# Performance work log

Hardware: AMD Instinct MI355X
Metric: run time of the kernel (lower is better)

## Reference

```python
import jax, jax.numpy as jnp
import numpy as np

MLP_WIDTH = 256
NUM_FREQS = 10


def _posenc(x):
    # [x, sin(pi x), cos(pi x), sin(2pi x), cos(2pi x), ...] -> last dim 2*(1+2*NUM_FREQS)=42
    freqs = (2.0 ** jnp.arange(NUM_FREQS, dtype=x.dtype)) * jnp.pi
    parts = [x]
    for f in freqs:
        parts.append(jnp.sin(x * f))
        parts.append(jnp.cos(x * f))
    return jnp.concatenate(parts, axis=-1)


def _bilinear_sample(grid, coords):
    # grid: [B,Hl,Wl,C]; coords: [N,2] in [-1,1], col0=y(dim H), col1=x(dim W).
    # Equivalent to map_coordinates(order=1, mode='reflect') since rescaled coords
    # lie in [0, size-1]; at the upper edge the out-of-range tap has zero weight,
    # so clipping == reflecting.
    Hl, Wl = grid.shape[1], grid.shape[2]
    y = (coords[:, 0] + 1.0) * 0.5 * (Hl - 1)
    x = (coords[:, 1] + 1.0) * 0.5 * (Wl - 1)
    y0 = jnp.floor(y)
    x0 = jnp.floor(x)
    wy = (y - y0)[None, :, None]  # [1,N,1]
    wx = (x - x0)[None, :, None]
    y0i = jnp.clip(y0.astype(jnp.int32), 0, Hl - 1)
    x0i = jnp.clip(x0.astype(jnp.int32), 0, Wl - 1)
    y1i = jnp.clip(y0i + 1, 0, Hl - 1)
    x1i = jnp.clip(x0i + 1, 0, Wl - 1)
    g00 = grid[:, y0i, x0i]  # [B,N,C]
    g01 = grid[:, y0i, x1i]
    g10 = grid[:, y1i, x0i]
    g11 = grid[:, y1i, x1i]
    top = g00 * (1 - wx) + g01 * wx
    bot = g10 * (1 - wx) + g11 * wx
    return top * (1 - wy) + bot * wy


def _forward(feature_grid, context_vector, coords,
             Wc, bc, W0, b0, W1, b1, W2, b2, W3, b3, Wout, bout):
    B, H, W, C = feature_grid.shape
    enc = _posenc(coords)  # [N,42]
    pyramid = [feature_grid] + [
        jax.image.resize(feature_grid, (B, H // 2 ** i, W // 2 ** i, C), 'bilinear')
        for i in range(1, 3)
    ]
    sampled = [_bilinear_sample(g, coords) for g in pyramid]  # each [B,N,C]
    feats = jnp.concatenate(sampled, axis=-1)  # [B,N,3C]
    enc_tiled = jnp.broadcast_to(enc[None], (B,) + enc.shape)
    h = jnp.concatenate([enc_tiled, feats], axis=-1)  # [B,N,42+3C]
    # FiLM projection (shared across all MLP layers, as in the flax module)
    ctx = context_vector @ Wc + bc  # [B, 2*MLP_WIDTH]
    gamma = ctx[:, None, :MLP_WIDTH] + 1.0
    beta = ctx[:, None, MLP_WIDTH:]
    for Wl_, bl_ in ((W0, b0), (W1, b1), (W2, b2), (W3, b3)):
        h = h @ Wl_ + bl_
        h = h * gamma + beta
        h = jax.nn.gelu(h)  # approximate=True, matches flax nn.gelu
    return jnp.tanh(h @ Wout + bout)  # [B,N,3]


def setup_inputs() -> dict:
    key = jax.random.key(0)
    ks = jax.random.split(key, 16)
    B, H, W, C = 8, 64, 64, 64
    N = 16384
    enc_dim = 2 * (1 + 2 * NUM_FREQS)  # 42
    in_dim = enc_dim + 3 * C  # 234
    s = lambda d: 1.0 / np.sqrt(d)
    return {
        'feature_grid': jax.random.normal(ks[0], (B, H, W, C), jnp.float32),
        'context_vector': jax.random.normal(ks[1], (B, C), jnp.float32),
        'coords': jax.random.uniform(ks[2], (N, 2), jnp.float32, -1.0, 1.0),
        'Wc': jax.random.normal(ks[3], (C, 2 * MLP_WIDTH), jnp.float32) * s(C),
        'bc': jnp.zeros((2 * MLP_WIDTH,), jnp.float32),
        'W0': jax.random.normal(ks[4], (in_dim, MLP_WIDTH), jnp.float32) * s(in_dim),
        'b0': jnp.zeros((MLP_WIDTH,), jnp.float32),
        'W1': jax.random.normal(ks[5], (MLP_WIDTH, MLP_WIDTH), jnp.float32) * s(MLP_WIDTH),
        'b1': jnp.zeros((MLP_WIDTH,), jnp.float32),
        'W2': jax.random.normal(ks[6], (MLP_WIDTH, MLP_WIDTH), jnp.float32) * s(MLP_WIDTH),
        'b2': jnp.zeros((MLP_WIDTH,), jnp.float32),
        'W3': jax.random.normal(ks[7], (MLP_WIDTH, MLP_WIDTH), jnp.float32) * s(MLP_WIDTH),
        'b3': jnp.zeros((MLP_WIDTH,), jnp.float32),
        'Wout': jax.random.normal(ks[8], (MLP_WIDTH, 3), jnp.float32) * 0.01,
        'bout': jnp.zeros((3,), jnp.float32),
    }


def reference(feature_grid, context_vector, coords,
              Wc, bc, W0, b0, W1, b1, W2, b2, W3, b3, Wout, bout):
    return _forward(feature_grid, context_vector, coords,
                    Wc, bc, W0, b0, W1, b1, W2, b2, W3, b3, Wout, bout)
```

## Files before the change

kernel.cpp:

```cpp
#include <hip/hip_runtime.h>
#include <math.h>

typedef _Float16 f16x8 __attribute__((ext_vector_type(8)));
typedef float f32x4 __attribute__((ext_vector_type(4)));
typedef float f32x16 __attribute__((ext_vector_type(16)));
typedef unsigned short us8 __attribute__((ext_vector_type(8)));
typedef unsigned short us4 __attribute__((ext_vector_type(4)));

#define PI_F 3.14159265358979323846f

__device__ __forceinline__ unsigned short f2h(float f){
  _Float16 hi = (_Float16)f;
  return __builtin_bit_cast(unsigned short, hi);
}

__device__ __forceinline__ float fast_gelu(float v){
  float u2 = v * v;
  float z  = v * fmaf(u2, 0.03567740814f, 0.7978845608f);
  float e  = __builtin_amdgcn_exp2f(z * 2.885390082f);
  float r  = __builtin_amdgcn_rcpf(e + 1.0f);
  return v - v * r;
}

__device__ __forceinline__ float fast_tanh(float v){
  float e = __builtin_amdgcn_exp2f(v * 2.885390082f);
  float r = __builtin_amdgcn_rcpf(e + 1.0f);
  return 1.0f - 2.0f * r;
}

#define ACOL(rr,cc) (((rr) << 8) + ((cc) ^ ((((rr) & 15)) << 3)))

#define LDW(ptr) __builtin_bit_cast(f16x8, *reinterpret_cast<const us8*>(ptr))

__global__ void pyr_kernel(const float* __restrict__ fg, float* __restrict__ out,
                           int Ho, int Wo, float inv_scale){
  int idx = blockIdx.x * blockDim.x + threadIdx.x;
  int total = 8 * Ho * Wo * 64;
  if (idx >= total) return;
  int c  = idx & 63;
  int xy = idx >> 6;
  int x  = xy % Wo;
  int y  = (xy / Wo) % Ho;
  int b  = xy / (Wo * Ho);
  float cyc = inv_scale * (y + 0.5f) - 0.5f;
  float cxc = inv_scale * (x + 0.5f) - 0.5f;
  int iy0 = (int)ceilf(cyc - inv_scale); if (iy0 < 0) iy0 = 0;
  int iy1 = (int)floorf(cyc + inv_scale); if (iy1 > 63) iy1 = 63;
  int ix0 = (int)ceilf(cxc - inv_scale); if (ix0 < 0) ix0 = 0;
  int ix1 = (int)floorf(cxc + inv_scale); if (ix1 > 63) ix1 = 63;
  float rinv = 1.0f / inv_scale;
  float wxs = 0.0f;
  for (int ix = ix0; ix <= ix1; ++ix){
    float w = 1.0f - fabsf(ix - cxc) * rinv;
    if (w > 0.0f) wxs += w;
  }
  float wys = 0.0f, acc = 0.0f;
  for (int iy = iy0; iy <= iy1; ++iy){
    float wy = 1.0f - fabsf(iy - cyc) * rinv;
    if (wy <= 0.0f) continue;
    wys += wy;
    const float* rowp = fg + (((b * 64) + iy) * 64) * 64 + c;
    for (int ix = ix0; ix <= ix1; ++ix){
      float wx = 1.0f - fabsf(ix - cxc) * rinv;
      if (wx <= 0.0f) continue;
      acc += wy * wx * rowp[ix * 64];
    }
  }
  out[idx] = acc / (wys * wxs);
}

__global__ void pe_kernel(const float* __restrict__ coords,
                          unsigned short* __restrict__ peh){
  int idx = blockIdx.x * 256 + threadIdx.x;
  if (idx >= 16384 * 12) return;
  int n = idx / 12, slot = idx % 12;
  const float cy = coords[2 * n], cx = coords[2 * n + 1];
  if (slot == 0){
    peh[n * 48 + 0] = f2h(cy);
    peh[n * 48 + 1] = f2h(cx);
  } else if (slot <= 10){
    int i = slot - 1;
    float f = PI_F * (float)(1 << i);
    float sy, cyv, sx, cxv;
    sincosf(cy * f, &sy, &cyv);
    sincosf(cx * f, &sx, &cxv);
    peh[n * 48 + 2 + 4 * i] = f2h(sy);
    peh[n * 48 + 3 + 4 * i] = f2h(sx);
    peh[n * 48 + 4 + 4 * i] = f2h(cyv);
    peh[n * 48 + 5 + 4 * i] = f2h(cxv);
  } else {
#pragma unroll
    for (int j = 42; j < 48; ++j) peh[n * 48 + j] = 0;
  }
}

__global__ void prep_wt(const float* __restrict__ W0, const float* __restrict__ W1,
                        const float* __restrict__ W2, const float* __restrict__ W3,
                        unsigned short* __restrict__ WTh){
  int idx = blockIdx.x * 256 + threadIdx.x;
  int l    = idx >> 16;
  int rem  = idx & 65535;
  int cfg  = rem >> 13;
  int ks   = (rem >> 9) & 15;
  int lane = (rem >> 3) & 63;
  int e    = idx & 7;
  int col  = cfg * 32 + (lane & 31);
  int k    = ks * 16 + (lane >> 5) * 8 + e;
  float v;
  if (l == 0){
    int row; bool valid;
    if (k < 42)                 { row = k;     valid = true; }
    else if (k >= 48 && k < 240){ row = k - 6; valid = true; }
    else                        { row = 0;     valid = false; }
    v = valid ? W0[row * 256 + col] : 0.0f;
  } else {
    const float* W = (l == 1) ? W1 : ((l == 2) ? W2 : W3);
    v = W[k * 256 + col];
  }
  WTh[idx] = f2h(v);
}

__global__ void prep_misc(const float* __restrict__ cv, const float* __restrict__ Wc,
                          const float* __restrict__ bc, const float* __restrict__ Wout,
                          float* __restrict__ gamma, float* __restrict__ beta,
                          unsigned short* __restrict__ WoT){
  int idx = blockIdx.x * 256 + threadIdx.x;
  if (idx < 4096){
    int b = idx >> 9, j = idx & 511;
    float a = bc[j];
    for (int c = 0; c < 64; ++c) a += cv[b * 64 + c] * Wc[c * 512 + j];
    if (j < 256) gamma[b * 256 + j] = a + 1.0f;
    else         beta[b * 256 + (j - 256)] = a;
  } else {
    int j = idx - 4096;
    int ks = j >> 9, lane = (j >> 3) & 63, e = j & 7;
    int col = lane & 15;
    int k = ks * 32 + (lane >> 4) * 8 + e;
    float v = (col < 3) ? Wout[k * 3 + col] : 0.0f;
    WoT[j] = f2h(v);
  }
}

__global__ __launch_bounds__(512, 2)
void dec_main(const float* __restrict__ fg, const float* __restrict__ coords,
              const float* __restrict__ p1, const float* __restrict__ p2,
              const unsigned short* __restrict__ WTh,
              const unsigned short* __restrict__ WoT,
              const unsigned short* __restrict__ peh,
              const float* __restrict__ gamma, const float* __restrict__ beta,
              const float* __restrict__ b0, const float* __restrict__ b1,
              const float* __restrict__ b2, const float* __restrict__ b3,
              const float* __restrict__ bout, float* __restrict__ out){
  __shared__ __align__(16) unsigned short Ah0[80 * 256];
  __shared__ __align__(16) unsigned short Ah1[80 * 256];
  __shared__ __align__(16) float Pgs[256];
  __shared__ __align__(16) float C2s[4][256];

  const int t  = threadIdx.x;
  const int bi = blockIdx.x >> 8;
  const int n0 = (blockIdx.x & 255) * 64;

  const int lane = t & 63;
  const int wv   = t >> 6;
  const int l15  = lane & 15;
  const int lg   = lane >> 4;
  const int l31  = lane & 31;
  const int lhi  = lane >> 5;

  const int rg   = wv >> 2;
  const int cg   = wv & 3;
  const int arow = rg * 32 + l31;

  const int b0off = (cg * 2)     * 8192 + lane * 8;
  const int b1off = (cg * 2 + 1) * 8192 + lane * 8;

  if (t < 256){
    const float gm = gamma[bi * 256 + t];
    const float bt = beta[bi * 256 + t];
    Pgs[t] = gm;
    C2s[0][t] = fmaf(b0[t], gm, bt);
    C2s[1][t] = fmaf(b1[t], gm, bt);
    C2s[2][t] = fmaf(b2[t], gm, bt);
    C2s[3][t] = fmaf(b3[t], gm, bt);

    const int r = t >> 2, q = t & 3;
    const int n = n0 + r;
    const float cy = coords[2 * n], cx = coords[2 * n + 1];

    if (q == 0){
      if (peh){
        const unsigned short* ph = peh + (size_t)n * 48;
#pragma unroll
        for (int u = 0; u < 6; ++u){
          us8 vh = *reinterpret_cast<const us8*>(ph + u * 8);
          *reinterpret_cast<us8*>(&Ah0[ACOL(r, u * 8)]) = vh;
        }
      } else {
        float e[48];
        e[0] = cy; e[1] = cx;
#pragma unroll
        for (int i = 0; i < 10; ++i){
          float f = PI_F * (float)(1 << i);
          float sy, cyv, sx, cxv;
          sincosf(cy * f, &sy, &cyv);
          sincosf(cx * f, &sx, &cxv);
          e[2 + 4 * i] = sy;
          e[3 + 4 * i] = sx;
          e[4 + 4 * i] = cyv;
          e[5 + 4 * i] = cxv;
        }
#pragma unroll
        for (int j = 42; j < 48; ++j) e[j] = 0.0f;
#pragma unroll
        for (int u = 0; u < 6; ++u){
          us8 vh;
#pragma unroll
          for (int j = 0; j < 8; ++j) vh[j] = f2h(e[8 * u + j]);
          *reinterpret_cast<us8*>(&Ah0[ACOL(r, u * 8)]) = vh;
        }
      }
    }
    if (q == 1){
      us8 z = {0,0,0,0,0,0,0,0};
      *reinterpret_cast<us8*>(&Ah0[ACOL(r, 240)]) = z;
      *reinterpret_cast<us8*>(&Ah0[ACOL(r, 248)]) = z;
    }

#pragma unroll
    for (int L = 0; L < 3; ++L){
      const int HL = 64 >> L;
      const float* g = (L == 0) ? fg : ((L == 1) ? p1 : p2);
      float yy = (cy + 1.0f) * 0.5f * (HL - 1);
      float xx = (cx + 1.0f) * 0.5f * (HL - 1);
      float y0f = floorf(yy), x0f = floorf(xx);
      float wy = yy - y0f, wx = xx - x0f;
      int y0 = (int)y0f, x0 = (int)x0f;
      y0 = min(max(y0, 0), HL - 1); x0 = min(max(x0, 0), HL - 1);
      int y1 = min(y0 + 1, HL - 1), x1 = min(x0 + 1, HL - 1);
      const int c0 = q * 16;
      const float* g00 = g + (((bi * HL + y0) * HL) + x0) * 64 + c0;
      const float* g01 = g + (((bi * HL + y0) * HL) + x1) * 64 + c0;
      const float* g10 = g + (((bi * HL + y1) * HL) + x0) * 64 + c0;
      const float* g11 = g + (((bi * HL + y1) * HL) + x1) * 64 + c0;
      float w00 = (1 - wy) * (1 - wx), w01 = (1 - wy) * wx;
      float w10 = wy * (1 - wx),       w11 = wy * wx;
      float o[16];
#pragma unroll
      for (int u = 0; u < 4; ++u){
        float4 v0 = *reinterpret_cast<const float4*>(g00 + 4 * u);
        float4 v1 = *reinterpret_cast<const float4*>(g01 + 4 * u);
        float4 v2 = *reinterpret_cast<const float4*>(g10 + 4 * u);
        float4 v3 = *reinterpret_cast<const float4*>(g11 + 4 * u);
        o[4*u+0] = w00*v0.x + w01*v1.x + w10*v2.x + w11*v3.x;
        o[4*u+1] = w00*v0.y + w01*v1.y + w10*v2.y + w11*v3.y;
        o[4*u+2] = w00*v0.z + w01*v1.z + w10*v2.z + w11*v3.z;
        o[4*u+3] = w00*v0.w + w01*v1.w + w10*v2.w + w11*v3.w;
      }
      us8 h0, h1;
#pragma unroll
      for (int j = 0; j < 8; ++j){
        h0[j] = f2h(o[j]);
        h1[j] = f2h(o[8 + j]);
      }
      const int colb = 48 + 64 * L + 16 * q;
      *reinterpret_cast<us8*>(&Ah0[ACOL(r, colb)])     = h0;
      *reinterpret_cast<us8*>(&Ah0[ACOL(r, colb + 8)]) = h1;
    }
  }

  f16x8 bf0[8], bf1[8];
#pragma unroll
  for (int p = 0; p < 8; ++p){
    bf0[p] = LDW(WTh + b0off + p * 512);
    bf1[p] = LDW(WTh + b1off + p * 512);
  }
  __syncthreads();

#pragma unroll
  for (int l = 0; l < 4; ++l){
    const unsigned short* Rh   = (l & 1) ? Ah1 : Ah0;
    unsigned short*       Wh_t = (l & 1) ? Ah0 : Ah1;
    const unsigned short* Wcur = WTh + l * 65536;
    const unsigned short* Wnxt = WTh + (l + 1) * 65536;

    f32x16 accA, accB;
#pragma unroll
    for (int j = 0; j < 16; ++j){ accA[j] = 0.0f; accB[j] = 0.0f; }

#pragma unroll
    for (int ks = 0; ks < 16; ++ks){
      const int cur = ks & 7;
      const int kc = ks * 16 + lhi * 8;
      f16x8 ah  = LDW(&Rh[ACOL(arow, kc)]);
      f16x8 b0v = bf0[cur], b1v = bf1[cur];
      if (ks < 8){
        bf0[cur] = LDW(Wcur + b0off + (ks + 8) * 512);
        bf1[cur] = LDW(Wcur + b1off + (ks + 8) * 512);
      } else if (l < 3){
        bf0[cur] = LDW(Wnxt + b0off + (ks - 8) * 512);
        bf1[cur] = LDW(Wnxt + b1off + (ks - 8) * 512);
      }
      accA = __builtin_amdgcn_mfma_f32_32x32x16_f16(b0v, ah, accA, 0, 0, 0);
      accB = __builtin_amdgcn_mfma_f32_32x32x16_f16(b1v, ah, accB, 0, 0, 0);
    }

#define EPI32(ACC, CF) do { \
      _Pragma("unroll") \
      for (int g = 0; g < 4; ++g){ \
        const int colb = cg * 64 + (CF) * 32 + 4 * lhi + 8 * g; \
        const float4 gm4 = *reinterpret_cast<const float4*>(&Pgs[colb]); \
        const float4 c24 = *reinterpret_cast<const float4*>(&C2s[l][colb]); \
        us4 hh; \
        { float v = fmaf((ACC)[4*g+0], gm4.x, c24.x); hh[0] = f2h(fast_gelu(v)); } \
        { float v = fmaf((ACC)[4*g+1], gm4.y, c24.y); hh[1] = f2h(fast_gelu(v)); } \
        { float v = fmaf((ACC)[4*g+2], gm4.z, c24.z); hh[2] = f2h(fast_gelu(v)); } \
        { float v = fmaf((ACC)[4*g+3], gm4.w, c24.w); hh[3] = f2h(fast_gelu(v)); } \
        *reinterpret_cast<us4*>(&Wh_t[ACOL(arow, colb)]) = hh; \
      } } while(0)
    EPI32(accA, 0);
    EPI32(accB, 1);
#undef EPI32
    __syncthreads();
  }

  if (wv < 4){
    f32x4 ao = (f32x4){0.0f, 0.0f, 0.0f, 0.0f};
#pragma unroll
    for (int ks = 0; ks < 8; ++ks){
      const int kc = ks * 32 + lg * 8;
      f16x8 va = LDW(&Ah0[ACOL(wv * 16 + l15, kc)]);
      f16x8 vb = LDW(&WoT[(ks * 64 + lane) * 8]);
      ao = __builtin_amdgcn_mfma_f32_16x16x32_f16(va, vb, ao, 0, 0, 0);
    }
    if (l15 < 3){
      const float bo = bout[l15];
#pragma unroll
      for (int rg2 = 0; rg2 < 4; ++rg2){
        const int row = wv * 16 + lg * 4 + rg2;
        out[((size_t)bi * 16384 + n0 + row) * 3 + l15] = fast_tanh(ao[rg2] + bo);
      }
    }
  }
}

extern "C" void kernel_launch(void* const* d_in, const int* in_sizes, int n_in,
                              void* d_out, int out_size, void* d_ws, size_t ws_size,
                              hipStream_t stream){
  (void)in_sizes; (void)n_in; (void)out_size;
  const float* fg     = (const float*)d_in[0];
  const float* cv     = (const float*)d_in[1];
  const float* coords = (const float*)d_in[2];
  const float* Wc     = (const float*)d_in[3];
  const float* bc     = (const float*)d_in[4];
  const float* W0     = (const float*)d_in[5];
  const float* b0     = (const float*)d_in[6];
  const float* W1     = (const float*)d_in[7];
  const float* b1     = (const float*)d_in[8];
  const float* W2     = (const float*)d_in[9];
  const float* b2     = (const float*)d_in[10];
  const float* W3     = (const float*)d_in[11];
  const float* b3     = (const float*)d_in[12];
  const float* Wout   = (const float*)d_in[13];
  const float* bout   = (const float*)d_in[14];

  char* ws = (char*)d_ws;
  float*          p1    = (float*)(ws);
  float*          p2    = (float*)(ws + 2097152);
  unsigned short* WTh   = (unsigned short*)(ws + 2621440);
  unsigned short* WoT   = (unsigned short*)(ws + 3670016);
  float*          gam   = (float*)(ws + 3678208);
  float*          bet   = (float*)(ws + 3686400);
  const size_t PEH_OFF = 4194304, PE_END = 5767168;
  bool use_pe = (ws_size >= PE_END);
  unsigned short* PEh = use_pe ? (unsigned short*)(ws + PEH_OFF) : nullptr;
  float* outp = (float*)d_out;

  pyr_kernel<<<dim3(2048), dim3(256), 0, stream>>>(fg, p1, 32, 32, 2.0f);
  pyr_kernel<<<dim3(512),  dim3(256), 0, stream>>>(fg, p2, 16, 16, 4.0f);
  prep_wt  <<<dim3(1024),  dim3(256), 0, stream>>>(W0, W1, W2, W3, WTh);
  prep_misc<<<dim3(32),    dim3(256), 0, stream>>>(cv, Wc, bc, Wout, gam, bet, WoT);
  if (use_pe)
    pe_kernel<<<dim3(768), dim3(256), 0, stream>>>(coords, PEh);
  dec_main <<<dim3(2048),  dim3(512), 0, stream>>>(fg, coords, p1, p2, WTh, WoT,
                                                   PEh,
                                                   gam, bet, b0, b1, b2, b3, bout, outp);
}
```

Measured before the change: 187.5 us.

## Keep MLP activations in registers with per-wave full-width tiles and larger blocks

```diff
diff --git a/kernel.cpp b/kernel.cpp
--- a/kernel.cpp
+++ b/kernel.cpp
@@ -105,15 +105,17 @@
   int lane = (rem >> 3) & 63;
   int e    = idx & 7;
   int col  = cfg * 32 + (lane & 31);
-  int k    = ks * 16 + (lane >> 5) * 8 + e;
   float v;
   if (l == 0){
+    int k = ks * 16 + (lane >> 5) * 8 + e;
     int row; bool valid;
     if (k < 42)                 { row = k;     valid = true; }
     else if (k >= 48 && k < 240){ row = k - 6; valid = true; }
     else                        { row = 0;     valid = false; }
     v = valid ? W0[row * 256 + col] : 0.0f;
   } else {
+    int c_in = ks >> 1, gp = ks & 1;
+    int k = c_in * 32 + gp * 16 + (e >> 2) * 8 + (lane >> 5) * 4 + (e & 3);
     const float* W = (l == 1) ? W1 : ((l == 2) ? W2 : W3);
     v = W[k * 256 + col];
   }
@@ -151,14 +153,13 @@
               const float* __restrict__ b0, const float* __restrict__ b1,
               const float* __restrict__ b2, const float* __restrict__ b3,
               const float* __restrict__ bout, float* __restrict__ out){
-  __shared__ __align__(16) unsigned short Ah0[80 * 256];
-  __shared__ __align__(16) unsigned short Ah1[80 * 256];
+  __shared__ __align__(16) unsigned short T0[256 * 256];
   __shared__ __align__(16) float Pgs[256];
   __shared__ __align__(16) float C2s[4][256];
 
   const int t  = threadIdx.x;
-  const int bi = blockIdx.x >> 8;
-  const int n0 = (blockIdx.x & 255) * 64;
+  const int bi = blockIdx.x >> 6;
+  const int n0 = (blockIdx.x & 63) * 256;
 
   const int lane = t & 63;
   const int wv   = t >> 6;
@@ -166,13 +167,12 @@
   const int lg   = lane >> 4;
   const int l31  = lane & 31;
   const int lhi  = lane >> 5;
-
-  const int rg   = wv >> 2;
-  const int cg   = wv & 3;
-  const int arow = rg * 32 + l31;
-
-  const int b0off = (cg * 2)     * 8192 + lane * 8;
-  const int b1off = (cg * 2 + 1) * 8192 + lane * 8;
+  const int arow = wv * 32 + l31;
+
+  f16x8 Bc[8];
+#pragma unroll
+  for (int c = 0; c < 8; ++c)
+    Bc[c] = LDW(WTh + c * 8192 + lane * 8);
 
   if (t < 256){
     const float gm = gamma[bi * 256 + t];
@@ -182,8 +182,11 @@
     C2s[1][t] = fmaf(b1[t], gm, bt);
     C2s[2][t] = fmaf(b2[t], gm, bt);
     C2s[3][t] = fmaf(b3[t], gm, bt);
-
-    const int r = t >> 2, q = t & 3;
+  }
+
+#pragma unroll
+  for (int pass = 0; pass < 2; ++pass){
+    const int r = pass * 128 + (t >> 2), q = t & 3;
     const int n = n0 + r;
     const float cy = coords[2 * n], cx = coords[2 * n + 1];
 
@@ -193,7 +196,7 @@
 #pragma unroll
         for (int u = 0; u < 6; ++u){
           us8 vh = *reinterpret_cast<const us8*>(ph + u * 8);
-          *reinterpret_cast<us8*>(&Ah0[ACOL(r, u * 8)]) = vh;
+          *reinterpret_cast<us8*>(&T0[ACOL(r, u * 8)]) = vh;
         }
       } else {
         float e[48];
@@ -216,14 +219,14 @@
           us8 vh;
 #pragma unroll
           for (int j = 0; j < 8; ++j) vh[j] = f2h(e[8 * u + j]);
-          *reinterpret_cast<us8*>(&Ah0[ACOL(r, u * 8)]) = vh;
+          *reinterpret_cast<us8*>(&T0[ACOL(r, u * 8)]) = vh;
         }
       }
     }
     if (q == 1){
       us8 z = {0,0,0,0,0,0,0,0};
-      *reinterpret_cast<us8*>(&Ah0[ACOL(r, 240)]) = z;
-      *reinterpret_cast<us8*>(&Ah0[ACOL(r, 248)]) = z;
+      *reinterpret_cast<us8*>(&T0[ACOL(r, 240)]) = z;
+      *reinterpret_cast<us8*>(&T0[ACOL(r, 248)]) = z;
     }
 
 #pragma unroll
@@ -263,72 +266,104 @@
         h1[j] = f2h(o[8 + j]);
       }
       const int colb = 48 + 64 * L + 16 * q;
-      *reinterpret_cast<us8*>(&Ah0[ACOL(r, colb)])     = h0;
-      *reinterpret_cast<us8*>(&Ah0[ACOL(r, colb + 8)]) = h1;
-    }
-  }
-
-  f16x8 bf0[8], bf1[8];
-#pragma unroll
-  for (int p = 0; p < 8; ++p){
-    bf0[p] = LDW(WTh + b0off + p * 512);
-    bf1[p] = LDW(WTh + b1off + p * 512);
+      *reinterpret_cast<us8*>(&T0[ACOL(r, colb)])     = h0;
+      *reinterpret_cast<us8*>(&T0[ACOL(r, colb + 8)]) = h1;
+    }
   }
   __syncthreads();
 
-#pragma unroll
-  for (int l = 0; l < 4; ++l){
-    const unsigned short* Rh   = (l & 1) ? Ah1 : Ah0;
-    unsigned short*       Wh_t = (l & 1) ? Ah0 : Ah1;
-    const unsigned short* Wcur = WTh + l * 65536;
-    const unsigned short* Wnxt = WTh + (l + 1) * 65536;
-
-    f32x16 accA, accB;
-#pragma unroll
-    for (int j = 0; j < 16; ++j){ accA[j] = 0.0f; accB[j] = 0.0f; }
-
-#pragma unroll
-    for (int ks = 0; ks < 16; ++ks){
-      const int cur = ks & 7;
-      const int kc = ks * 16 + lhi * 8;
-      f16x8 ah  = LDW(&Rh[ACOL(arow, kc)]);
-      f16x8 b0v = bf0[cur], b1v = bf1[cur];
-      if (ks < 8){
-        bf0[cur] = LDW(Wcur + b0off + (ks + 8) * 512);
-        bf1[cur] = LDW(Wcur + b1off + (ks + 8) * 512);
-      } else if (l < 3){
-        bf0[cur] = LDW(Wnxt + b0off + (ks - 8) * 512);
-        bf1[cur] = LDW(Wnxt + b1off + (ks - 8) * 512);
-      }
-      accA = __builtin_amdgcn_mfma_f32_32x32x16_f16(b0v, ah, accA, 0, 0, 0);
-      accB = __builtin_amdgcn_mfma_f32_32x32x16_f16(b1v, ah, accB, 0, 0, 0);
-    }
-
-#define EPI32(ACC, CF) do { \
+  f32x16 acc[8];
+  f16x8 actA[16], actB[16];
+
+#define EPI_REG(LIDX, AOUT) do { \
+    _Pragma("unroll") \
+    for (int c = 0; c < 8; ++c){ \
       _Pragma("unroll") \
-      for (int g = 0; g < 4; ++g){ \
-        const int colb = cg * 64 + (CF) * 32 + 4 * lhi + 8 * g; \
-        const float4 gm4 = *reinterpret_cast<const float4*>(&Pgs[colb]); \
-        const float4 c24 = *reinterpret_cast<const float4*>(&C2s[l][colb]); \
-        us4 hh; \
-        { float v = fmaf((ACC)[4*g+0], gm4.x, c24.x); hh[0] = f2h(fast_gelu(v)); } \
-        { float v = fmaf((ACC)[4*g+1], gm4.y, c24.y); hh[1] = f2h(fast_gelu(v)); } \
-        { float v = fmaf((ACC)[4*g+2], gm4.z, c24.z); hh[2] = f2h(fast_gelu(v)); } \
-        { float v = fmaf((ACC)[4*g+3], gm4.w, c24.w); hh[3] = f2h(fast_gelu(v)); } \
-        *reinterpret_cast<us4*>(&Wh_t[ACOL(arow, colb)]) = hh; \
-      } } while(0)
-    EPI32(accA, 0);
-    EPI32(accB, 1);
-#undef EPI32
-    __syncthreads();
-  }
-
-  if (wv < 4){
+      for (int gp = 0; gp < 2; ++gp){ \
+        const int cb2 = c * 32 + 16 * gp + 4 * lhi; \
+        const float4 gmA = *reinterpret_cast<const float4*>(&Pgs[cb2]); \
+        const float4 c2A = *reinterpret_cast<const float4*>(&C2s[LIDX][cb2]); \
+        const float4 gmB = *reinterpret_cast<const float4*>(&Pgs[cb2 + 8]); \
+        const float4 c2B = *reinterpret_cast<const float4*>(&C2s[LIDX][cb2 + 8]); \
+        us8 hv; \
+        hv[0] = f2h(fast_gelu(fmaf(acc[c][8*gp+0], gmA.x, c2A.x))); \
+        hv[1] = f2h(fast_gelu(fmaf(acc[c][8*gp+1], gmA.y, c2A.y))); \
+        hv[2] = f2h(fast_gelu(fmaf(acc[c][8*gp+2], gmA.z, c2A.z))); \
+        hv[3] = f2h(fast_gelu(fmaf(acc[c][8*gp+3], gmA.w, c2A.w))); \
+        hv[4] = f2h(fast_gelu(fmaf(acc[c][8*gp+4], gmB.x, c2B.x))); \
+        hv[5] = f2h(fast_gelu(fmaf(acc[c][8*gp+5], gmB.y, c2B.y))); \
+        hv[6] = f2h(fast_gelu(fmaf(acc[c][8*gp+6], gmB.z, c2B.z))); \
+        hv[7] = f2h(fast_gelu(fmaf(acc[c][8*gp+7], gmB.w, c2B.w))); \
+        (AOUT)[c * 2 + gp] = __builtin_bit_cast(f16x8, hv); \
+      } \
+    } } while(0)
+
+#pragma unroll
+  for (int j = 0; j < 16; ++j){
+#pragma unroll
+    for (int c = 0; c < 8; ++c) acc[c][j] = 0.0f;
+  }
+#pragma unroll
+  for (int ks = 0; ks < 16; ++ks){
+    f16x8 ah = LDW(&T0[ACOL(arow, ks * 16 + lhi * 8)]);
+#pragma unroll
+    for (int c = 0; c < 8; ++c){
+      f16x8 b = Bc[c];
+      if (ks < 15) Bc[c] = LDW(WTh + c * 8192 + (ks + 1) * 512 + lane * 8);
+      else         Bc[c] = LDW(WTh + 65536 + c * 8192 + lane * 8);
+      acc[c] = __builtin_amdgcn_mfma_f32_32x32x16_f16(b, ah, acc[c], 0, 0, 0);
+    }
+  }
+  EPI_REG(0, actA);
+
+#define LAYER_REG(LIDX, AIN, AOUT) do { \
+    _Pragma("unroll") \
+    for (int j = 0; j < 16; ++j){ \
+      _Pragma("unroll") \
+      for (int c = 0; c < 8; ++c) acc[c][j] = 0.0f; \
+    } \
+    _Pragma("unroll") \
+    for (int ks = 0; ks < 16; ++ks){ \
+      f16x8 ah = (AIN)[ks]; \
+      _Pragma("unroll") \
+      for (int c = 0; c < 8; ++c){ \
+        f16x8 b = Bc[c]; \
+        if (ks < 15) \
+          Bc[c] = LDW(WTh + (LIDX) * 65536 + c * 8192 + (ks + 1) * 512 + lane * 8); \
+        else if ((LIDX) < 3) \
+          Bc[c] = LDW(WTh + ((LIDX) + 1) * 65536 + c * 8192 + lane * 8); \
+        acc[c] = __builtin_amdgcn_mfma_f32_32x32x16_f16(b, ah, acc[c], 0, 0, 0); \
+      } \
+    } \
+    EPI_REG(LIDX, AOUT); \
+  } while(0)
+
+  LAYER_REG(1, actA, actB);
+  LAYER_REG(2, actB, actA);
+  LAYER_REG(3, actA, actB);
+
+#pragma unroll
+  for (int c = 0; c < 8; ++c){
+#pragma unroll
+    for (int gp = 0; gp < 2; ++gp){
+      us8 v = __builtin_bit_cast(us8, actB[c * 2 + gp]);
+      us4 lo4, hi4;
+      lo4[0]=v[0]; lo4[1]=v[1]; lo4[2]=v[2]; lo4[3]=v[3];
+      hi4[0]=v[4]; hi4[1]=v[5]; hi4[2]=v[6]; hi4[3]=v[7];
+      const int cb2 = c * 32 + 16 * gp + 4 * lhi;
+      *reinterpret_cast<us4*>(&T0[ACOL(arow, cb2)])     = lo4;
+      *reinterpret_cast<us4*>(&T0[ACOL(arow, cb2 + 8)]) = hi4;
+    }
+  }
+  __syncthreads();
+
+#pragma unroll
+  for (int s = 0; s < 2; ++s){
     f32x4 ao = (f32x4){0.0f, 0.0f, 0.0f, 0.0f};
 #pragma unroll
     for (int ks = 0; ks < 8; ++ks){
       const int kc = ks * 32 + lg * 8;
-      f16x8 va = LDW(&Ah0[ACOL(wv * 16 + l15, kc)]);
+      f16x8 va = LDW(&T0[ACOL(wv * 32 + s * 16 + l15, kc)]);
       f16x8 vb = LDW(&WoT[(ks * 64 + lane) * 8]);
       ao = __builtin_amdgcn_mfma_f32_16x16x32_f16(va, vb, ao, 0, 0, 0);
     }
@@ -336,7 +371,7 @@
       const float bo = bout[l15];
 #pragma unroll
       for (int rg2 = 0; rg2 < 4; ++rg2){
-        const int row = wv * 16 + lg * 4 + rg2;
+        const int row = wv * 32 + s * 16 + lg * 4 + rg2;
         out[((size_t)bi * 16384 + n0 + row) * 3 + l15] = fast_tanh(ao[rg2] + bo);
       }
     }
@@ -381,7 +416,7 @@
   prep_misc<<<dim3(32),    dim3(256), 0, stream>>>(cv, Wc, bc, Wout, gam, bet, WoT);
   if (use_pe)
     pe_kernel<<<dim3(768), dim3(256), 0, stream>>>(coords, PEh);
-  dec_main <<<dim3(2048),  dim3(512), 0, stream>>>(fg, coords, p1, p2, WTh, WoT,
+  dec_main <<<dim3(512),   dim3(512), 0, stream>>>(fg, coords, p1, p2, WTh, WoT,
                                                    PEh,
                                                    gam, bet, b0, b1, b2, b3, bout, outp);
 }
```

New measurement: 346.7 us. 84.9% more time.
